# Kernel tuning notes

Hardware: AMD Instinct MI355X
Metric: run time of the kernel (lower is better)

The kernel has to match this reference:

```python
import jax, jax.numpy as jnp
import numpy as np

NUM_BINS = 32
NUM_HEADS = 4
CHANNELS = 128
HEAD_DIM = CHANNELS // NUM_HEADS
SCALE = HEAD_DIM ** -0.5
BN_EPS = 1e-5


def setup_inputs() -> dict:
    key = jax.random.key(0)
    ks = jax.random.split(key, 8)
    B = 8192
    x = jax.random.normal(ks[0], (B, CHANNELS, NUM_BINS), dtype=jnp.float32)
    qkv_w = jax.random.normal(ks[1], (3 * CHANNELS, CHANNELS), dtype=jnp.float32) * (1.0 / np.sqrt(CHANNELS))
    qkv_b = jax.random.normal(ks[2], (3 * CHANNELS,), dtype=jnp.float32) * 0.01
    out_w = jax.random.normal(ks[3], (CHANNELS, CHANNELS), dtype=jnp.float32) * (1.0 / np.sqrt(CHANNELS))
    out_b = jax.random.normal(ks[4], (CHANNELS,), dtype=jnp.float32) * 0.01
    rel_pos_emb = jax.random.normal(ks[5], (2 * NUM_BINS - 1, NUM_HEADS), dtype=jnp.float32) * 0.02
    gamma = jnp.ones((CHANNELS,), dtype=jnp.float32)
    beta = jnp.zeros((CHANNELS,), dtype=jnp.float32)
    return {"x": x, "qkv_w": qkv_w, "qkv_b": qkv_b, "out_w": out_w,
            "out_b": out_b, "rel_pos_emb": rel_pos_emb, "gamma": gamma, "beta": beta}


def _rel_pos_bias(rel_pos_emb, n):
    # pos_idx[i,j] = (j - i) + num_bins - 1, clamped
    pos = jnp.arange(n)
    idx = jnp.clip(pos[None, :] - pos[:, None] + NUM_BINS - 1, 0, 2 * NUM_BINS - 2)
    bias = rel_pos_emb[idx]            # [n, n, H]
    return jnp.transpose(bias, (2, 0, 1))  # [H, n, n]


def reference(x, qkv_w, qkv_b, out_w, out_b, rel_pos_emb, gamma, beta):
    B, C, N = x.shape
    residual = x
    # 1x1 conv == per-position matmul over channels
    qkv = jnp.einsum('oc,bcn->bon', qkv_w, x) + qkv_b[None, :, None]  # [B, 3C, N]
    q, k, v = jnp.split(qkv, 3, axis=1)
    def heads(t):  # [B, C, N] -> [B, H, N, D]
        return jnp.transpose(t.reshape(B, NUM_HEADS, HEAD_DIM, N), (0, 1, 3, 2))
    q, k, v = heads(q), heads(k), heads(v)
    attn = jnp.einsum('bhnd,bhmd->bhnm', q, k) * SCALE
    attn = attn + _rel_pos_bias(rel_pos_emb, N)[None]  # [B, H, N, N]
    attn = jax.nn.softmax(attn, axis=-1)
    out = jnp.einsum('bhnm,bhmd->bhnd', attn, v)       # [B, H, N, D]
    out = jnp.transpose(out, (0, 1, 3, 2)).reshape(B, C, N)
    out = jnp.einsum('oc,bcn->bon', out_w, out) + out_b[None, :, None]
    out = out + residual
    # BatchNorm1d (training-mode batch stats, biased variance), per-channel over (B, N)
    mean = jnp.mean(out, axis=(0, 2), keepdims=True)
    var = jnp.mean((out - mean) ** 2, axis=(0, 2), keepdims=True)
    out = (out - mean) / jnp.sqrt(var + BN_EPS)
    out = out * gamma[None, :, None] + beta[None, :, None]
    return out
```

## Files before the change

kernel.cpp:

```cpp
#include <hip/hip_runtime.h>
#include <hip/hip_bf16.h>

typedef unsigned short u16;
typedef __bf16 bf16x8 __attribute__((ext_vector_type(8)));
typedef float f32x4 __attribute__((ext_vector_type(4)));

#define CH 128
#define NB 32
#define NH 4
#define HD 32
#define SCALE_F 0.17677669529663687f

__device__ __forceinline__ u16 f2b(float f) {
  union { float f; unsigned u; } v; v.f = f;
  unsigned r = v.u + 0x7fffu + ((v.u >> 16) & 1u);
  return (u16)(r >> 16);
}

__global__ void prep_kernel(const float* __restrict__ qw, const float* __restrict__ ow,
                            u16* __restrict__ wq, u16* __restrict__ wo,
                            float* __restrict__ stats) {
  int t = blockIdx.x * 256 + threadIdx.x;
  if (t < 49152) wq[t] = f2b(qw[t]);
  if (t < 16384) wo[t] = f2b(ow[t]);
  if (t < 8192)  stats[t] = 0.0f;
}

__global__ __launch_bounds__(256, 3) void attn_kernel(
    const float* __restrict__ x, const u16* __restrict__ wq,
    const float* __restrict__ qkv_b, const u16* __restrict__ wo,
    const float* __restrict__ out_b, const float* __restrict__ rel,
    float* __restrict__ out, float* __restrict__ stats) {

  __shared__ __attribute__((aligned(16))) u16 sXt[32 * 128];
  __shared__ __attribute__((aligned(16))) u16 sQKt[32 * 256];
  __shared__ __attribute__((aligned(16))) u16 sVn[128 * 40];
  __shared__ __attribute__((aligned(16))) u16 sP[4 * 32 * 40];

  const int tid = threadIdx.x;
  const int w    = tid >> 6;
  const int lane = tid & 63;
  const int g    = lane >> 4;
  const int l15  = lane & 15;
  const int b    = blockIdx.x;
  const float* xb = x + (size_t)b * (CH * NB);

  #pragma unroll
  for (int it = 0; it < 4; ++it) {
    int id = it * 256 + tid;
    int c = id >> 3, n4 = id & 7;
    const float4 v = *(const float4*)(xb + c * NB + n4 * 4);
    float vv[4] = {v.x, v.y, v.z, v.w};
    #pragma unroll
    for (int j = 0; j < 4; ++j) {
      int n = n4 * 4 + j;
      sXt[(n * 128 + c) ^ ((n & 7) << 3)] = f2b(vv[j]);
    }
  }
  __syncthreads();

  {
    f32x4 acc[6][2];
    #pragma unroll
    for (int mi = 0; mi < 6; ++mi)
      #pragma unroll
      for (int ct = 0; ct < 2; ++ct)
        acc[mi][ct] = (f32x4){0.f, 0.f, 0.f, 0.f};

    #pragma unroll
    for (int kk = 0; kk < 4; ++kk) {
      bf16x8 bfr[2];
      #pragma unroll
      for (int ct = 0; ct < 2; ++ct) {
        int n = ct * 16 + l15;
        bfr[ct] = *(const bf16x8*)&sXt[(n * 128 + kk * 32 + 8 * g) ^ ((n & 7) << 3)];
      }
      #pragma unroll
      for (int mi = 0; mi < 6; ++mi) {
        int row = 96 * w + mi * 16 + l15;
        bf16x8 afr = *(const bf16x8*)&wq[row * 128 + kk * 32 + 8 * g];
        acc[mi][0] = __builtin_amdgcn_mfma_f32_16x16x32_bf16(afr, bfr[0], acc[mi][0], 0, 0, 0);
        acc[mi][1] = __builtin_amdgcn_mfma_f32_16x16x32_bf16(afr, bfr[1], acc[mi][1], 0, 0, 0);
      }
    }
    #pragma unroll
    for (int mi = 0; mi < 6; ++mi) {
      #pragma unroll
      for (int r = 0; r < 4; ++r) {
        int o = 96 * w + mi * 16 + 4 * g + r;
        float qb = qkv_b[o];
        #pragma unroll
        for (int ct = 0; ct < 2; ++ct) {
          int n = ct * 16 + l15;
          u16 hv = f2b(acc[mi][ct][r] + qb);
          if (o < 256) sQKt[(n * 256 + o) ^ ((n & 7) << 3)] = hv;
          else         sVn[(o - 256) * 40 + n] = hv;
        }
      }
    }
  }
  __syncthreads();

  {
    const int h = w;
    const f32x4 zf = (f32x4){0.f, 0.f, 0.f, 0.f};
    bf16x8 qf[2], kf[2];
    #pragma unroll
    for (int t2 = 0; t2 < 2; ++t2) {
      int n = t2 * 16 + l15;
      qf[t2] = *(const bf16x8*)&sQKt[(n * 256 + h * 32 + 8 * g) ^ ((n & 7) << 3)];
      kf[t2] = *(const bf16x8*)&sQKt[(n * 256 + 128 + h * 32 + 8 * g) ^ ((n & 7) << 3)];
    }
    f32x4 sacc[2][2];
    #pragma unroll
    for (int tn = 0; tn < 2; ++tn)
      #pragma unroll
      for (int tm = 0; tm < 2; ++tm)
        sacc[tn][tm] = __builtin_amdgcn_mfma_f32_16x16x32_bf16(qf[tn], kf[tm], zf, 0, 0, 0);

    u16* sPw = &sP[w * 32 * 40];
    #pragma unroll
    for (int tn = 0; tn < 2; ++tn) {
      #pragma unroll
      for (int r = 0; r < 4; ++r) {
        int n = tn * 16 + 4 * g + r;
        float v0 = sacc[tn][0][r] * SCALE_F + rel[(l15      - n + 31) * 4 + h];
        float v1 = sacc[tn][1][r] * SCALE_F + rel[(16 + l15 - n + 31) * 4 + h];
        float mx = fmaxf(v0, v1);
        #pragma unroll
        for (int msk = 1; msk < 16; msk <<= 1) mx = fmaxf(mx, __shfl_xor(mx, msk));
        float e0 = __expf(v0 - mx), e1 = __expf(v1 - mx);
        float sm = e0 + e1;
        #pragma unroll
        for (int msk = 1; msk < 16; msk <<= 1) sm += __shfl_xor(sm, msk);
        float rinv = 1.0f / sm;
        sPw[n * 40 + l15]      = f2b(e0 * rinv);
        sPw[n * 40 + 16 + l15] = f2b(e1 * rinv);
      }
    }
    __syncthreads();

    bf16x8 pf[2], vf[2];
    #pragma unroll
    for (int t2 = 0; t2 < 2; ++t2) {
      pf[t2] = *(const bf16x8*)&sPw[(t2 * 16 + l15) * 40 + 8 * g];
      vf[t2] = *(const bf16x8*)&sVn[(h * 32 + t2 * 16 + l15) * 40 + 8 * g];
    }
    f32x4 oacc[2][2];
    #pragma unroll
    for (int tn = 0; tn < 2; ++tn)
      #pragma unroll
      for (int td = 0; td < 2; ++td)
        oacc[tn][td] = __builtin_amdgcn_mfma_f32_16x16x32_bf16(pf[tn], vf[td], zf, 0, 0, 0);

    #pragma unroll
    for (int tn = 0; tn < 2; ++tn)
      #pragma unroll
      for (int td = 0; td < 2; ++td)
        #pragma unroll
        for (int r = 0; r < 4; ++r) {
          int n = tn * 16 + 4 * g + r;
          int c = h * 32 + td * 16 + l15;
          sXt[(n * 128 + c) ^ ((n & 7) << 3)] = f2b(oacc[tn][td][r]);
        }
  }
  __syncthreads();

  {
    f32x4 pacc[2][2];
    #pragma unroll
    for (int mi = 0; mi < 2; ++mi)
      #pragma unroll
      for (int ct = 0; ct < 2; ++ct)
        pacc[mi][ct] = (f32x4){0.f, 0.f, 0.f, 0.f};

    #pragma unroll
    for (int kk = 0; kk < 4; ++kk) {
      bf16x8 bfr[2];
      #pragma unroll
      for (int ct = 0; ct < 2; ++ct) {
        int n = ct * 16 + l15;
        bfr[ct] = *(const bf16x8*)&sXt[(n * 128 + kk * 32 + 8 * g) ^ ((n & 7) << 3)];
      }
      #pragma unroll
      for (int mi = 0; mi < 2; ++mi) {
        int row = 32 * w + mi * 16 + l15;
        bf16x8 afr = *(const bf16x8*)&wo[row * 128 + kk * 32 + 8 * g];
        #pragma unroll
        for (int ct = 0; ct < 2; ++ct)
          pacc[mi][ct] = __builtin_amdgcn_mfma_f32_16x16x32_bf16(afr, bfr[ct], pacc[mi][ct], 0, 0, 0);
      }
    }

    float* ob = out + (size_t)b * (CH * NB);
    #pragma unroll
    for (int mi = 0; mi < 2; ++mi) {
      #pragma unroll
      for (int r = 0; r < 4; ++r) {
        int o = 32 * w + mi * 16 + 4 * g + r;
        float bias = out_b[o];
        float ssum = 0.f, ssq = 0.f;
        #pragma unroll
        for (int ct = 0; ct < 2; ++ct) {
          int n = ct * 16 + l15;
          float val = pacc[mi][ct][r] + bias + xb[o * NB + n];
          ob[o * NB + n] = val;
          ssum += val; ssq += val * val;
        }
        #pragma unroll
        for (int msk = 1; msk < 16; msk <<= 1) {
          ssum += __shfl_xor(ssum, msk);
          ssq  += __shfl_xor(ssq, msk);
        }
        if (l15 == 0) {
          atomicAdd(&stats[(b & 31) * 128 + o], ssum);
          atomicAdd(&stats[4096 + (b & 31) * 128 + o], ssq);
        }
      }
    }
  }
}

__global__ void bnstats_kernel(const float* __restrict__ stats,
                               const float* __restrict__ gamma,
                               const float* __restrict__ beta,
                               float* __restrict__ sc, float* __restrict__ sh,
                               float invM) {
  int c = threadIdx.x;
  if (c >= 128) return;
  float s = 0.f, q = 0.f;
  #pragma unroll 8
  for (int i = 0; i < 32; ++i) {
    s += stats[i * 128 + c];
    q += stats[4096 + i * 128 + c];
  }
  float mean = s * invM;
  float var  = q * invM - mean * mean;
  float rstd = rsqrtf(var + 1e-5f);
  float a = gamma[c] * rstd;
  sc[c] = a;
  sh[c] = beta[c] - mean * a;
}

__global__ __launch_bounds__(256) void bnapply_kernel(float* __restrict__ out,
                                                      const float* __restrict__ sc,
                                                      const float* __restrict__ sh,
                                                      int n4total) {
  int i = blockIdx.x * 256 + threadIdx.x;
  int stride = gridDim.x * 256;
  for (; i < n4total; i += stride) {
    int c = (i >> 3) & 127;
    float a = sc[c], d = sh[c];
    float4 v = ((float4*)out)[i];
    v.x = v.x * a + d;
    v.y = v.y * a + d;
    v.z = v.z * a + d;
    v.w = v.w * a + d;
    ((float4*)out)[i] = v;
  }
}

extern "C" void kernel_launch(void* const* d_in, const int* in_sizes, int n_in,
                              void* d_out, int out_size, void* d_ws, size_t ws_size,
                              hipStream_t stream) {
  const float* x     = (const float*)d_in[0];
  const float* qkv_w = (const float*)d_in[1];
  const float* qkv_b = (const float*)d_in[2];
  const float* out_w = (const float*)d_in[3];
  const float* out_b = (const float*)d_in[4];
  const float* rel   = (const float*)d_in[5];
  const float* gamma = (const float*)d_in[6];
  const float* beta  = (const float*)d_in[7];
  float* out = (float*)d_out;

  const int B = in_sizes[0] / (CH * NB);

  u16* wq = (u16*)d_ws;
  u16* wo = wq + 49152;
  float* stats = (float*)(wo + 16384);
  float* sc = stats + 8192;
  float* sh = sc + 128;

  prep_kernel<<<192, 256, 0, stream>>>(qkv_w, out_w, wq, wo, stats);
  attn_kernel<<<B, 256, 0, stream>>>(x, wq, qkv_b, wo, out_b, rel, out, stats);
  bnstats_kernel<<<1, 128, 0, stream>>>(stats, gamma, beta, sc, sh, 1.0f / (float)(B * NB));
  bnapply_kernel<<<2048, 256, 0, stream>>>(out, sc, sh, out_size / 4);
}
```

Baseline: 471.1 us.

## Assign one head per warp for QKV projection to drop block-wide syncs

Each warp now computes the Q, K and V projection rows for its own head, reading x directly from global memory into MFMA fragments instead of staging a transposed bf16 copy in shared memory. Per-warp V and P buffers let the attention stage proceed without block barriers, leaving only the two syncs around the output projection. It also raises the occupancy hint to 4 blocks and fetches relative-position bias through lane shuffles. The cost is uncoalesced strided global reads of x, repeated by every warp, and more register pressure under the tighter launch bound.

```diff
diff --git a/kernel.cpp b/kernel.cpp
--- a/kernel.cpp
+++ b/kernel.cpp
@@ -7,8 +7,6 @@
 
 #define CH 128
 #define NB 32
-#define NH 4
-#define HD 32
 #define SCALE_F 0.17677669529663687f
 
 __device__ __forceinline__ u16 f2b(float f) {
@@ -26,196 +24,184 @@
   if (t < 8192)  stats[t] = 0.0f;
 }
 
-__global__ __launch_bounds__(256, 3) void attn_kernel(
+__global__ __launch_bounds__(256, 4) void attn_kernel(
     const float* __restrict__ x, const u16* __restrict__ wq,
     const float* __restrict__ qkv_b, const u16* __restrict__ wo,
     const float* __restrict__ out_b, const float* __restrict__ rel,
     float* __restrict__ out, float* __restrict__ stats) {
 
-  __shared__ __attribute__((aligned(16))) u16 sXt[32 * 128];
   __shared__ __attribute__((aligned(16))) u16 sQKt[32 * 256];
-  __shared__ __attribute__((aligned(16))) u16 sVn[128 * 40];
-  __shared__ __attribute__((aligned(16))) u16 sP[4 * 32 * 40];
+  __shared__ __attribute__((aligned(16))) u16 sVn[4][32 * 40];
+  __shared__ __attribute__((aligned(16))) u16 sPO[4][32 * 40];
 
   const int tid = threadIdx.x;
-  const int w    = tid >> 6;
-  const int lane = tid & 63;
-  const int g    = lane >> 4;
-  const int l15  = lane & 15;
-  const int b    = blockIdx.x;
+  const int w = tid >> 6, lane = tid & 63;
+  const int g = lane >> 4, l15 = lane & 15;
+  const int b = blockIdx.x, h = w;
   const float* xb = x + (size_t)b * (CH * NB);
-
-  #pragma unroll
-  for (int it = 0; it < 4; ++it) {
-    int id = it * 256 + tid;
-    int c = id >> 3, n4 = id & 7;
-    const float4 v = *(const float4*)(xb + c * NB + n4 * 4);
-    float vv[4] = {v.x, v.y, v.z, v.w};
-    #pragma unroll
-    for (int j = 0; j < 4; ++j) {
-      int n = n4 * 4 + j;
-      sXt[(n * 128 + c) ^ ((n & 7) << 3)] = f2b(vv[j]);
-    }
-  }
+  const f32x4 zf = {0.f, 0.f, 0.f, 0.f};
+
+  const float relv = rel[(lane < 63 ? lane : 62) * 4 + h];
+
+  f32x4 acc[6][2];
+  #pragma unroll
+  for (int tt = 0; tt < 6; ++tt)
+    #pragma unroll
+    for (int ct = 0; ct < 2; ++ct) acc[tt][ct] = zf;
+
+  #pragma unroll
+  for (int kk = 0; kk < 4; ++kk) {
+    bf16x8 bfr[2];
+    #pragma unroll
+    for (int ct = 0; ct < 2; ++ct) {
+      float xv[8];
+      #pragma unroll
+      for (int j = 0; j < 8; ++j)
+        xv[j] = xb[(kk * 32 + 8 * g + j) * NB + 16 * ct + l15];
+      union { bf16x8 v; unsigned u[4]; } uu;
+      #pragma unroll
+      for (int m = 0; m < 4; ++m)
+        uu.u[m] = (unsigned)f2b(xv[2 * m]) | ((unsigned)f2b(xv[2 * m + 1]) << 16);
+      bfr[ct] = uu.v;
+    }
+    #pragma unroll
+    for (int tt = 0; tt < 6; ++tt) {
+      const int part = tt >> 1, td = tt & 1;
+      const int row = part * 128 + h * 32 + 16 * td + l15;
+      bf16x8 afr = *(const bf16x8*)&wq[row * 128 + kk * 32 + 8 * g];
+      acc[tt][0] = __builtin_amdgcn_mfma_f32_16x16x32_bf16(afr, bfr[0], acc[tt][0], 0, 0, 0);
+      acc[tt][1] = __builtin_amdgcn_mfma_f32_16x16x32_bf16(afr, bfr[1], acc[tt][1], 0, 0, 0);
+    }
+  }
+
+  #pragma unroll
+  for (int tt = 0; tt < 6; ++tt) {
+    const int part = tt >> 1, td = tt & 1;
+    #pragma unroll
+    for (int r = 0; r < 4; ++r) {
+      const int d = 16 * td + 4 * g + r;
+      const int orow = part * 128 + h * 32 + d;
+      const float bias = qkv_b[orow];
+      #pragma unroll
+      for (int ct = 0; ct < 2; ++ct) {
+        const int n = 16 * ct + l15;
+        const u16 hv = f2b(acc[tt][ct][r] + bias);
+        if (part < 2) sQKt[(n * 256 + orow) ^ ((n & 7) << 3)] = hv;
+        else          sVn[w][d * 40 + n] = hv;
+      }
+    }
+  }
+
+  bf16x8 qf[2], kf[2];
+  #pragma unroll
+  for (int t2 = 0; t2 < 2; ++t2) {
+    const int n = 16 * t2 + l15;
+    qf[t2] = *(const bf16x8*)&sQKt[(n * 256 + h * 32 + 8 * g) ^ ((n & 7) << 3)];
+    kf[t2] = *(const bf16x8*)&sQKt[(n * 256 + 128 + h * 32 + 8 * g) ^ ((n & 7) << 3)];
+  }
+  f32x4 sacc[2][2];
+  #pragma unroll
+  for (int tn = 0; tn < 2; ++tn)
+    #pragma unroll
+    for (int tm = 0; tm < 2; ++tm)
+      sacc[tn][tm] = __builtin_amdgcn_mfma_f32_16x16x32_bf16(qf[tn], kf[tm], zf, 0, 0, 0);
+
+  u16* sPw = sPO[w];
+  #pragma unroll
+  for (int tn = 0; tn < 2; ++tn) {
+    #pragma unroll
+    for (int r = 0; r < 4; ++r) {
+      const int n = 16 * tn + 4 * g + r;
+      float v0 = sacc[tn][0][r] * SCALE_F + __shfl(relv, l15 - n + 31);
+      float v1 = sacc[tn][1][r] * SCALE_F + __shfl(relv, 16 + l15 - n + 31);
+      float mx = fmaxf(v0, v1);
+      #pragma unroll
+      for (int msk = 1; msk < 16; msk <<= 1) mx = fmaxf(mx, __shfl_xor(mx, msk));
+      float e0 = __expf(v0 - mx), e1 = __expf(v1 - mx);
+      float sm = e0 + e1;
+      #pragma unroll
+      for (int msk = 1; msk < 16; msk <<= 1) sm += __shfl_xor(sm, msk);
+      const float ri = 1.0f / sm;
+      sPw[n * 40 + l15]      = f2b(e0 * ri);
+      sPw[n * 40 + 16 + l15] = f2b(e1 * ri);
+    }
+  }
+
+  bf16x8 pf[2], vf[2];
+  #pragma unroll
+  for (int t2 = 0; t2 < 2; ++t2) {
+    pf[t2] = *(const bf16x8*)&sPw[(16 * t2 + l15) * 40 + 8 * g];
+    vf[t2] = *(const bf16x8*)&sVn[w][(16 * t2 + l15) * 40 + 8 * g];
+  }
+  f32x4 oacc[2][2];
+  #pragma unroll
+  for (int tn = 0; tn < 2; ++tn)
+    #pragma unroll
+    for (int td = 0; td < 2; ++td)
+      oacc[tn][td] = __builtin_amdgcn_mfma_f32_16x16x32_bf16(pf[tn], vf[td], zf, 0, 0, 0);
+
   __syncthreads();
 
-  {
-    f32x4 acc[6][2];
-    #pragma unroll
-    for (int mi = 0; mi < 6; ++mi)
-      #pragma unroll
-      for (int ct = 0; ct < 2; ++ct)
-        acc[mi][ct] = (f32x4){0.f, 0.f, 0.f, 0.f};
-
-    #pragma unroll
-    for (int kk = 0; kk < 4; ++kk) {
-      bf16x8 bfr[2];
+  u16* sO = &sPO[0][0];
+  #pragma unroll
+  for (int tn = 0; tn < 2; ++tn)
+    #pragma unroll
+    for (int td = 0; td < 2; ++td)
+      #pragma unroll
+      for (int r = 0; r < 4; ++r) {
+        const int n = 16 * tn + 4 * g + r;
+        const int c = h * 32 + 16 * td + l15;
+        sO[(n * 128 + c) ^ ((n & 7) << 3)] = f2b(oacc[tn][td][r]);
+      }
+
+  __syncthreads();
+
+  f32x4 pacc[2][2];
+  #pragma unroll
+  for (int mi = 0; mi < 2; ++mi)
+    #pragma unroll
+    for (int ct = 0; ct < 2; ++ct) pacc[mi][ct] = zf;
+
+  #pragma unroll
+  for (int kk = 0; kk < 4; ++kk) {
+    bf16x8 bfr[2];
+    #pragma unroll
+    for (int ct = 0; ct < 2; ++ct) {
+      const int n = 16 * ct + l15;
+      bfr[ct] = *(const bf16x8*)&sO[(n * 128 + kk * 32 + 8 * g) ^ ((n & 7) << 3)];
+    }
+    #pragma unroll
+    for (int mi = 0; mi < 2; ++mi) {
+      const int row = 32 * w + 16 * mi + l15;
+      bf16x8 afr = *(const bf16x8*)&wo[row * 128 + kk * 32 + 8 * g];
+      pacc[mi][0] = __builtin_amdgcn_mfma_f32_16x16x32_bf16(afr, bfr[0], pacc[mi][0], 0, 0, 0);
+      pacc[mi][1] = __builtin_amdgcn_mfma_f32_16x16x32_bf16(afr, bfr[1], pacc[mi][1], 0, 0, 0);
+    }
+  }
+
+  float* ob = out + (size_t)b * (CH * NB);
+  #pragma unroll
+  for (int mi = 0; mi < 2; ++mi) {
+    #pragma unroll
+    for (int r = 0; r < 4; ++r) {
+      const int o = 32 * w + 16 * mi + 4 * g + r;
+      const float bias = out_b[o];
+      float ssum = 0.f, ssq = 0.f;
       #pragma unroll
       for (int ct = 0; ct < 2; ++ct) {
-        int n = ct * 16 + l15;
-        bfr[ct] = *(const bf16x8*)&sXt[(n * 128 + kk * 32 + 8 * g) ^ ((n & 7) << 3)];
-      }
-      #pragma unroll
-      for (int mi = 0; mi < 6; ++mi) {
-        int row = 96 * w + mi * 16 + l15;
-        bf16x8 afr = *(const bf16x8*)&wq[row * 128 + kk * 32 + 8 * g];
-        acc[mi][0] = __builtin_amdgcn_mfma_f32_16x16x32_bf16(afr, bfr[0], acc[mi][0], 0, 0, 0);
-        acc[mi][1] = __builtin_amdgcn_mfma_f32_16x16x32_bf16(afr, bfr[1], acc[mi][1], 0, 0, 0);
-      }
-    }
-    #pragma unroll
-    for (int mi = 0; mi < 6; ++mi) {
-      #pragma unroll
-      for (int r = 0; r < 4; ++r) {
-        int o = 96 * w + mi * 16 + 4 * g + r;
-        float qb = qkv_b[o];
-        #pragma unroll
-        for (int ct = 0; ct < 2; ++ct) {
-          int n = ct * 16 + l15;
-          u16 hv = f2b(acc[mi][ct][r] + qb);
-          if (o < 256) sQKt[(n * 256 + o) ^ ((n & 7) << 3)] = hv;
-          else         sVn[(o - 256) * 40 + n] = hv;
-        }
-      }
-    }
-  }
-  __syncthreads();
-
-  {
-    const int h = w;
-    const f32x4 zf = (f32x4){0.f, 0.f, 0.f, 0.f};
-    bf16x8 qf[2], kf[2];
-    #pragma unroll
-    for (int t2 = 0; t2 < 2; ++t2) {
-      int n = t2 * 16 + l15;
-      qf[t2] = *(const bf16x8*)&sQKt[(n * 256 + h * 32 + 8 * g) ^ ((n & 7) << 3)];
-      kf[t2] = *(const bf16x8*)&sQKt[(n * 256 + 128 + h * 32 + 8 * g) ^ ((n & 7) << 3)];
-    }
-    f32x4 sacc[2][2];
-    #pragma unroll
-    for (int tn = 0; tn < 2; ++tn)
-      #pragma unroll
-      for (int tm = 0; tm < 2; ++tm)
-        sacc[tn][tm] = __builtin_amdgcn_mfma_f32_16x16x32_bf16(qf[tn], kf[tm], zf, 0, 0, 0);
-
-    u16* sPw = &sP[w * 32 * 40];
-    #pragma unroll
-    for (int tn = 0; tn < 2; ++tn) {
-      #pragma unroll
-      for (int r = 0; r < 4; ++r) {
-        int n = tn * 16 + 4 * g + r;
-        float v0 = sacc[tn][0][r] * SCALE_F + rel[(l15      - n + 31) * 4 + h];
-        float v1 = sacc[tn][1][r] * SCALE_F + rel[(16 + l15 - n + 31) * 4 + h];
-        float mx = fmaxf(v0, v1);
-        #pragma unroll
-        for (int msk = 1; msk < 16; msk <<= 1) mx = fmaxf(mx, __shfl_xor(mx, msk));
-        float e0 = __expf(v0 - mx), e1 = __expf(v1 - mx);
-        float sm = e0 + e1;
-        #pragma unroll
-        for (int msk = 1; msk < 16; msk <<= 1) sm += __shfl_xor(sm, msk);
-        float rinv = 1.0f / sm;
-        sPw[n * 40 + l15]      = f2b(e0 * rinv);
-        sPw[n * 40 + 16 + l15] = f2b(e1 * rinv);
-      }
-    }
-    __syncthreads();
-
-    bf16x8 pf[2], vf[2];
-    #pragma unroll
-    for (int t2 = 0; t2 < 2; ++t2) {
-      pf[t2] = *(const bf16x8*)&sPw[(t2 * 16 + l15) * 40 + 8 * g];
-      vf[t2] = *(const bf16x8*)&sVn[(h * 32 + t2 * 16 + l15) * 40 + 8 * g];
-    }
-    f32x4 oacc[2][2];
-    #pragma unroll
-    for (int tn = 0; tn < 2; ++tn)
-      #pragma unroll
-      for (int td = 0; td < 2; ++td)
-        oacc[tn][td] = __builtin_amdgcn_mfma_f32_16x16x32_bf16(pf[tn], vf[td], zf, 0, 0, 0);
-
-    #pragma unroll
-    for (int tn = 0; tn < 2; ++tn)
-      #pragma unroll
-      for (int td = 0; td < 2; ++td)
-        #pragma unroll
-        for (int r = 0; r < 4; ++r) {
-          int n = tn * 16 + 4 * g + r;
-          int c = h * 32 + td * 16 + l15;
-          sXt[(n * 128 + c) ^ ((n & 7) << 3)] = f2b(oacc[tn][td][r]);
-        }
-  }
-  __syncthreads();
-
-  {
-    f32x4 pacc[2][2];
-    #pragma unroll
-    for (int mi = 0; mi < 2; ++mi)
-      #pragma unroll
-      for (int ct = 0; ct < 2; ++ct)
-        pacc[mi][ct] = (f32x4){0.f, 0.f, 0.f, 0.f};
-
-    #pragma unroll
-    for (int kk = 0; kk < 4; ++kk) {
-      bf16x8 bfr[2];
-      #pragma unroll
-      for (int ct = 0; ct < 2; ++ct) {
-        int n = ct * 16 + l15;
-        bfr[ct] = *(const bf16x8*)&sXt[(n * 128 + kk * 32 + 8 * g) ^ ((n & 7) << 3)];
-      }
-      #pragma unroll
-      for (int mi = 0; mi < 2; ++mi) {
-        int row = 32 * w + mi * 16 + l15;
-        bf16x8 afr = *(const bf16x8*)&wo[row * 128 + kk * 32 + 8 * g];
-        #pragma unroll
-        for (int ct = 0; ct < 2; ++ct)
-          pacc[mi][ct] = __builtin_amdgcn_mfma_f32_16x16x32_bf16(afr, bfr[ct], pacc[mi][ct], 0, 0, 0);
-      }
-    }
-
-    float* ob = out + (size_t)b * (CH * NB);
-    #pragma unroll
-    for (int mi = 0; mi < 2; ++mi) {
-      #pragma unroll
-      for (int r = 0; r < 4; ++r) {
-        int o = 32 * w + mi * 16 + 4 * g + r;
-        float bias = out_b[o];
-        float ssum = 0.f, ssq = 0.f;
-        #pragma unroll
-        for (int ct = 0; ct < 2; ++ct) {
-          int n = ct * 16 + l15;
-          float val = pacc[mi][ct][r] + bias + xb[o * NB + n];
-          ob[o * NB + n] = val;
-          ssum += val; ssq += val * val;
-        }
-        #pragma unroll
-        for (int msk = 1; msk < 16; msk <<= 1) {
-          ssum += __shfl_xor(ssum, msk);
-          ssq  += __shfl_xor(ssq, msk);
-        }
-        if (l15 == 0) {
-          atomicAdd(&stats[(b & 31) * 128 + o], ssum);
-          atomicAdd(&stats[4096 + (b & 31) * 128 + o], ssq);
-        }
+        const int n = 16 * ct + l15;
+        const float val = pacc[mi][ct][r] + bias + xb[o * NB + n];
+        ob[o * NB + n] = val;
+        ssum += val; ssq += val * val;
+      }
+      #pragma unroll
+      for (int msk = 1; msk < 16; msk <<= 1) {
+        ssum += __shfl_xor(ssum, msk);
+        ssq  += __shfl_xor(ssq, msk);
+      }
+      if (l15 == 0) {
+        atomicAdd(&stats[(b & 31) * 128 + o], ssum);
+        atomicAdd(&stats[4096 + (b & 31) * 128 + o], ssq);
       }
     }
   }
```

Measured after the change: 430.0 us. 8.7% less time.
